# Performance work log

Hardware: AMD Instinct MI355X
Metric: run time of the kernel (lower is better)

Reference implementation:

```python
import jax, jax.numpy as jnp
import numpy as np

NUM_HEADS = 16
HEAD_DIM = 128  # embed_dim 2048 / 16 heads


def setup_inputs() -> dict:
    key = jax.random.key(0)
    x = jax.random.normal(key, (2, 2048, 2048), dtype=jnp.float32)
    return {"x": x}


def reference(x):
    # EvoAttn forward: V-only causal self-attention (q = k = v = reshaped x).
    B, L, E = x.shape
    H, D = NUM_HEADS, HEAD_DIM
    v = x.reshape(B, L, H, D).transpose(0, 2, 1, 3)  # (B, H, L, D)
    scale = 1.0 / jnp.sqrt(jnp.asarray(D, dtype=x.dtype))
    scores = jnp.einsum("bhqd,bhkd->bhqk", v, v) * scale  # (B, H, L, L)
    causal = jnp.tril(jnp.ones((L, L), dtype=bool))
    scores = jnp.where(causal[None, None], scores, jnp.asarray(-jnp.inf, dtype=scores.dtype))
    p = jax.nn.softmax(scores, axis=-1)
    y = jnp.einsum("bhqk,bhkd->bhqd", p, v)  # (B, H, L, D)
    return y.transpose(0, 2, 1, 3).reshape(B, L, E)
```

## Files before the change

kernel.cpp:

```cpp
#include <hip/hip_runtime.h>
#include <hip/hip_bf16.h>


#define TL 2048
#define TE 2048
#define TD 128
#define KB 64
#define NTILES 32
#define TILE_B 16384
#define KV_REGION (32 * NTILES * TILE_B)
#define WS_NEED (2u * (unsigned)KV_REGION)

typedef __attribute__((ext_vector_type(8))) short bf16x8;
typedef __attribute__((ext_vector_type(4))) float f32x4;
typedef __attribute__((ext_vector_type(8))) unsigned short u16x8;
typedef __attribute__((ext_vector_type(4))) unsigned short u16x4;

#define SCALE_LOG2E 0.12751879f

__device__ __forceinline__ unsigned short f2bf(float f) {
  __hip_bfloat16 h = __float2bfloat16(f);
  return __builtin_bit_cast(unsigned short, h);
}

__device__ __forceinline__ f32x4 mfma16(bf16x8 a, bf16x8 b, f32x4 c) {
  return __builtin_amdgcn_mfma_f32_16x16x32_bf16(a, b, c, 0, 0, 0);
}

__device__ __forceinline__ void gl_lds16(const void* g, void* l) {
  __builtin_amdgcn_global_load_lds(
      (__attribute__((address_space(1))) void*)(g),
      (__attribute__((address_space(3))) void*)(l), 16, 0, 0);
}

__global__ void __launch_bounds__(256)
prepack(const float* __restrict__ x, char* __restrict__ wsb) {
  const int bid = blockIdx.x;
  const int kt = bid & 31;
  const int bh = bid >> 5;
  const int b = bh >> 4;
  const int h = bh & 15;
  const float* src = x + (size_t)b * TL * TE + h * TD + (size_t)kt * KB * TE;
  const int t = threadIdx.x;
  const int kr = (t >> 4) << 2;
  const int d0 = (t & 15) << 3;
  unsigned short c[4][8];
#pragma unroll
  for (int rr = 0; rr < 4; ++rr) {
    const float* p = src + (kr + rr) * TE + d0;
    const float4 a = *(const float4*)p;
    const float4 bb = *(const float4*)(p + 4);
    c[rr][0] = f2bf(a.x);  c[rr][1] = f2bf(a.y);  c[rr][2] = f2bf(a.z);  c[rr][3] = f2bf(a.w);
    c[rr][4] = f2bf(bb.x); c[rr][5] = f2bf(bb.y); c[rr][6] = f2bf(bb.z); c[rr][7] = f2bf(bb.w);
  }
  char* gkv = wsb + (size_t)bid * TILE_B;
  const int kt2 = kr >> 4;
  const int q0r = kr & 15;
  const int cc_ = (t & 15) >> 2;
  const int gg_ = (t & 15) & 3;
#pragma unroll
  for (int rr = 0; rr < 4; ++rr) {
    u16x8 o = {c[rr][0], c[rr][1], c[rr][2], c[rr][3],
               c[rr][4], c[rr][5], c[rr][6], c[rr][7]};
    const int off = (((kt2 * 4 + cc_) * 64 + gg_ * 16 + (q0r + rr)) << 4);
    *(u16x8*)(gkv + off) = o;
  }
  char* gkt = wsb + KV_REGION + (size_t)bid * TILE_B;
  const int half = kr >> 5;
  const int g = (kr >> 3) & 3;
  const int j0 = kr & 7;
#pragma unroll
  for (int cc = 0; cc < 8; ++cc) {
    const int d = d0 + cc;
    u16x4 o = {c[0][cc], c[1][cc], c[2][cc], c[3][cc]};
    const int off = (((half * 8 + (d >> 4)) * 64 + g * 16 + (d & 15)) << 4) + j0 * 2;
    *(u16x4*)(gkt + off) = o;
  }
}

__global__ void __launch_bounds__(256)
evo_attn2(const char* __restrict__ wsb, float* __restrict__ out) {
  __shared__ char smem[3 * TILE_B + 8192];

  const int t = threadIdx.x;
  const int lane = t & 63;
  const int w = t >> 6;
  const int g = lane >> 4;
  const int q15 = lane & 15;

  const int blk = blockIdx.x;
  const int bh = (blk & 7) * 4 + (blk >> 7);
  const int a = (blk >> 3) & 15;
  const int b = bh >> 4;
  const int h = bh & 15;

  const char* gkv = wsb + (size_t)bh * (NTILES * TILE_B);
  const char* gkt = wsb + KV_REGION + (size_t)bh * (NTILES * TILE_B);
  char* plw = smem + 3 * TILE_B + w * 2048;
  const char* kvtb = smem + 2 * TILE_B;
  const int l16 = lane * 16;

#define STAGE_KV(BUFI, KT)                                                 \
  {                                                                        \
    char* dst_ = smem + (BUFI) * TILE_B + (t >> 6) * 1024;                 \
    const char* src_ = gkv + (size_t)(KT) * TILE_B + t * 16;               \
    _Pragma("unroll")                                                      \
    for (int i_ = 0; i_ < 4; ++i_) gl_lds16(src_ + i_ * 4096, dst_ + i_ * 4096); \
  }
#define STAGE_KVT(KT)                                                      \
  {                                                                        \
    char* dst_ = smem + 2 * TILE_B + (t >> 6) * 1024;                      \
    const char* src_ = gkt + (size_t)(KT) * TILE_B + t * 16;               \
    _Pragma("unroll")                                                      \
    for (int i_ = 0; i_ < 4; ++i_) gl_lds16(src_ + i_ * 4096, dst_ + i_ * 4096); \
  }

#pragma unroll 1
  for (int seg = 0; seg < 2; ++seg) {
    const int qt = seg ? (31 - a) : a;
    const int nt = qt + 1;

    STAGE_KV(0, qt);
    if (nt > 1) STAGE_KV(1, 0);
    STAGE_KVT(qt);
    asm volatile("s_waitcnt vmcnt(0)" ::: "memory");
    __builtin_amdgcn_s_barrier();
    asm volatile("" ::: "memory");

    bf16x8 qf[4];
#pragma unroll
    for (int c = 0; c < 4; ++c)
      qf[c] = *(const bf16x8*)(smem + (w * 4 + c) * 1024 + l16);

    f32x4 acc[8];
#pragma unroll
    for (int dt = 0; dt < 8; ++dt) acc[dt] = (f32x4){0.f, 0.f, 0.f, 0.f};
    float mrun = -1e30f;
    float lrun = 0.f;

    for (int s = 0; s < nt; ++s) {
      if (s > 0) {
        asm volatile("s_waitcnt vmcnt(8)" ::: "memory");
        __builtin_amdgcn_s_barrier();
        asm volatile("" ::: "memory");
      }
      const char* kv = smem + (s & 1) * TILE_B;

      float sv[16];
      __builtin_amdgcn_s_setprio(1);
#pragma unroll
      for (int kt2 = 0; kt2 < 4; ++kt2) {
        f32x4 st = (f32x4){0.f, 0.f, 0.f, 0.f};
#pragma unroll
        for (int c = 0; c < 4; ++c) {
          bf16x8 kf = *(const bf16x8*)(kv + (kt2 * 4 + c) * 1024 + l16);
          st = mfma16(kf, qf[c], st);
        }
#pragma unroll
        for (int r = 0; r < 4; ++r) sv[kt2 * 4 + r] = st[r];
      }
      __builtin_amdgcn_s_setprio(0);

      if (s == 0) {
        const int qrel = 16 * w + q15;
#pragma unroll
        for (int kt2 = 0; kt2 < 4; ++kt2)
#pragma unroll
          for (int r = 0; r < 4; ++r)
            if (kt2 * 16 + g * 4 + r > qrel) sv[kt2 * 4 + r] = -1e30f;
      }

      float m0 = fmaxf(fmaxf(sv[0], sv[1]), fmaxf(sv[2], sv[3]));
      float m1 = fmaxf(fmaxf(sv[4], sv[5]), fmaxf(sv[6], sv[7]));
      float m2 = fmaxf(fmaxf(sv[8], sv[9]), fmaxf(sv[10], sv[11]));
      float m3 = fmaxf(fmaxf(sv[12], sv[13]), fmaxf(sv[14], sv[15]));
      float tmax = fmaxf(fmaxf(m0, m1), fmaxf(m2, m3));
      tmax = fmaxf(tmax, __shfl_xor(tmax, 16));
      tmax = fmaxf(tmax, __shfl_xor(tmax, 32));

      float pf[16];
      if (__all(tmax <= mrun)) {
        const float nmc = -mrun * SCALE_LOG2E;
#pragma unroll
        for (int i = 0; i < 16; ++i) pf[i] = exp2f(fmaf(sv[i], SCALE_LOG2E, nmc));
      } else {
        const float mnew = fmaxf(mrun, tmax);
        const float al = exp2f((mrun - mnew) * SCALE_LOG2E);
        mrun = mnew;
        const float nmc = -mnew * SCALE_LOG2E;
#pragma unroll
        for (int i = 0; i < 16; ++i) pf[i] = exp2f(fmaf(sv[i], SCALE_LOG2E, nmc));
        lrun *= al;
        float ar[4];
#pragma unroll
        for (int r = 0; r < 4; ++r) ar[r] = __shfl(al, g * 4 + r);
#pragma unroll
        for (int dt = 0; dt < 8; ++dt)
#pragma unroll
          for (int r = 0; r < 4; ++r) acc[dt][r] *= ar[r];
      }
      {
        float s01 = (pf[0] + pf[1]) + (pf[2] + pf[3]);
        float s23 = (pf[4] + pf[5]) + (pf[6] + pf[7]);
        float s45 = (pf[8] + pf[9]) + (pf[10] + pf[11]);
        float s67 = (pf[12] + pf[13]) + (pf[14] + pf[15]);
        lrun += (s01 + s23) + (s45 + s67);
      }

      {
        const int wb = q15 * 16 + (g & 1) * 8;
#pragma unroll
        for (int kt2 = 0; kt2 < 4; ++kt2) {
          u16x4 o = {f2bf(pf[kt2 * 4]), f2bf(pf[kt2 * 4 + 1]),
                     f2bf(pf[kt2 * 4 + 2]), f2bf(pf[kt2 * 4 + 3])};
          *(u16x4*)(plw + (kt2 * 2 + (g >> 1)) * 256 + wb) = o;
        }
      }
      asm volatile("s_waitcnt lgkmcnt(0)" ::: "memory");

      if (s > 0) {
        if (s + 1 < nt) asm volatile("s_waitcnt vmcnt(4)" ::: "memory");
        else            asm volatile("s_waitcnt vmcnt(0)" ::: "memory");
        __builtin_amdgcn_s_barrier();
        asm volatile("" ::: "memory");
      }

      bf16x8 pa0 = *(const bf16x8*)(plw + g * 256 + q15 * 16);
      bf16x8 pa1 = *(const bf16x8*)(plw + (4 + g) * 256 + q15 * 16);
      __builtin_amdgcn_s_setprio(1);
#pragma unroll
      for (int dt = 0; dt < 8; ++dt) {
        bf16x8 vb0 = *(const bf16x8*)(kvtb + dt * 1024 + l16);
        bf16x8 vb1 = *(const bf16x8*)(kvtb + (8 + dt) * 1024 + l16);
        acc[dt] = mfma16(pa0, vb0, acc[dt]);
        acc[dt] = mfma16(pa1, vb1, acc[dt]);
      }
      __builtin_amdgcn_s_setprio(0);

      __builtin_amdgcn_s_barrier();
      asm volatile("" ::: "memory");
      if (s + 1 < nt) STAGE_KVT(s);
      if (s + 2 < nt) STAGE_KV(s & 1, s + 1);
    }

    lrun += __shfl_xor(lrun, 16);
    lrun += __shfl_xor(lrun, 32);
    const float inv = 1.f / lrun;
    float ir[4];
#pragma unroll
    for (int r = 0; r < 4; ++r) ir[r] = __shfl(inv, g * 4 + r);

    float* ob = out + ((size_t)b * TL + qt * 64 + 16 * w) * TE + h * TD;
#pragma unroll
    for (int dt = 0; dt < 8; ++dt)
#pragma unroll
      for (int r = 0; r < 4; ++r)
        ob[(g * 4 + r) * TE + dt * 16 + q15] = acc[dt][r] * ir[r];

    __builtin_amdgcn_s_barrier();
    asm volatile("" ::: "memory");
  }
}

__device__ __forceinline__ bf16x8 ld256s(const unsigned short* base, int row, int inrow) {
  const int off = (row * 256 + inrow) ^ ((row & 7) << 4);
  return *(const bf16x8*)((const char*)base + off);
}
__device__ __forceinline__ bf16x8 ld128s(const unsigned short* base, int row, int inrow) {
  const int off = (row * 128 + inrow) ^ ((row & 7) << 4);
  return *(const bf16x8*)((const char*)base + off);
}

__device__ __forceinline__ void stage_tile_fb(const float* __restrict__ src,
                                              unsigned short* kv, unsigned short* kvt,
                                              int t) {
  const int kr = (t >> 4) << 2;
  const int d0 = (t & 15) << 3;
  unsigned short c[4][8];
#pragma unroll
  for (int rr = 0; rr < 4; ++rr) {
    const float* p = src + (kr + rr) * TE + d0;
    const float4 a = *(const float4*)p;
    const float4 b = *(const float4*)(p + 4);
    c[rr][0] = f2bf(a.x); c[rr][1] = f2bf(a.y); c[rr][2] = f2bf(a.z); c[rr][3] = f2bf(a.w);
    c[rr][4] = f2bf(b.x); c[rr][5] = f2bf(b.y); c[rr][6] = f2bf(b.z); c[rr][7] = f2bf(b.w);
  }
#pragma unroll
  for (int rr = 0; rr < 4; ++rr) {
    const int r = kr + rr;
    u16x8 o = {c[rr][0], c[rr][1], c[rr][2], c[rr][3],
               c[rr][4], c[rr][5], c[rr][6], c[rr][7]};
    const int off = (r * 256 + d0 * 2) ^ ((r & 7) << 4);
    *(u16x8*)((char*)kv + off) = o;
  }
#pragma unroll
  for (int cc = 0; cc < 8; ++cc) {
    const int d = d0 + cc;
    u16x4 o = {c[0][cc], c[1][cc], c[2][cc], c[3][cc]};
    const int off = (d * 128 + kr * 2) ^ ((d & 7) << 4);
    *(u16x4*)((char*)kvt + off) = o;
  }
}

__global__ void __launch_bounds__(256)
evo_attn(const float* __restrict__ x, float* __restrict__ out) {
  __shared__ unsigned short kv[KB * TD];
  __shared__ unsigned short kvt[TD * KB];
  __shared__ unsigned short pl[4 * 16 * KB];

  const int t = threadIdx.x;
  const int lane = t & 63;
  const int w = t >> 6;
  const int g = lane >> 4;
  const int q15 = lane & 15;

  const int bh = blockIdx.x & 31;
  const int qt = 31 - (blockIdx.x >> 5);
  const int b = bh >> 4;
  const int h = bh & 15;
  const float* xb = x + (size_t)b * TL * TE + h * TD;
  const int q0 = qt * KB;

  stage_tile_fb(xb + (size_t)q0 * TE, kv, kvt, t);
  __syncthreads();

  bf16x8 qf[4];
#pragma unroll
  for (int c = 0; c < 4; ++c)
    qf[c] = ld256s(kv, 16 * w + q15, c * 64 + g * 16);

  f32x4 acc[8];
#pragma unroll
  for (int dt = 0; dt < 8; ++dt) acc[dt] = (f32x4){0.f, 0.f, 0.f, 0.f};
  float mrun = -1e30f;
  float lrun = 0.f;
  unsigned short* plw = pl + w * (16 * KB);

  for (int s = 0; s <= qt; ++s) {
    if (s > 0) {
      __syncthreads();
      stage_tile_fb(xb + (size_t)(s - 1) * KB * TE, kv, kvt, t);
      __syncthreads();
    }
    float sv[16];
#pragma unroll
    for (int kt2 = 0; kt2 < 4; ++kt2) {
      f32x4 st = (f32x4){0.f, 0.f, 0.f, 0.f};
#pragma unroll
      for (int c = 0; c < 4; ++c) {
        bf16x8 kf = ld256s(kv, kt2 * 16 + q15, c * 64 + g * 16);
        st = mfma16(kf, qf[c], st);
      }
#pragma unroll
      for (int r = 0; r < 4; ++r) sv[kt2 * 4 + r] = st[r] * SCALE_LOG2E;
    }
    if (s == 0) {
      const int qrel = 16 * w + q15;
#pragma unroll
      for (int kt2 = 0; kt2 < 4; ++kt2)
#pragma unroll
        for (int r = 0; r < 4; ++r)
          if (kt2 * 16 + g * 4 + r > qrel) sv[kt2 * 4 + r] = -1e30f;
    }
    float tmax = sv[0];
#pragma unroll
    for (int i = 1; i < 16; ++i) tmax = fmaxf(tmax, sv[i]);
    tmax = fmaxf(tmax, __shfl_xor(tmax, 16));
    tmax = fmaxf(tmax, __shfl_xor(tmax, 32));
    const float mnew = fmaxf(mrun, tmax);
    const float al = exp2f(mrun - mnew);
    mrun = mnew;
    float psum = 0.f;
    unsigned short pb[16];
#pragma unroll
    for (int i = 0; i < 16; ++i) {
      const float p = exp2f(sv[i] - mnew);
      psum += p;
      pb[i] = f2bf(p);
    }
    lrun = lrun * al + psum;
#pragma unroll
    for (int kt2 = 0; kt2 < 4; ++kt2) {
      u16x4 o = {pb[kt2 * 4], pb[kt2 * 4 + 1], pb[kt2 * 4 + 2], pb[kt2 * 4 + 3]};
      const int off = (q15 * 128 + kt2 * 32 + g * 8) ^ ((q15 & 7) << 4);
      *(u16x4*)((char*)plw + off) = o;
    }
    asm volatile("s_waitcnt lgkmcnt(0)" ::: "memory");
    float ar[4];
#pragma unroll
    for (int r = 0; r < 4; ++r) ar[r] = __shfl(al, g * 4 + r);
#pragma unroll
    for (int dt = 0; dt < 8; ++dt)
#pragma unroll
      for (int r = 0; r < 4; ++r) acc[dt][r] *= ar[r];
    bf16x8 pa0 = ld128s(plw, q15, g * 16);
    bf16x8 pa1 = ld128s(plw, q15, 64 + g * 16);
#pragma unroll
    for (int dt = 0; dt < 8; ++dt) {
      bf16x8 vb0 = ld128s(kvt, dt * 16 + q15, g * 16);
      bf16x8 vb1 = ld128s(kvt, dt * 16 + q15, 64 + g * 16);
      acc[dt] = mfma16(pa0, vb0, acc[dt]);
      acc[dt] = mfma16(pa1, vb1, acc[dt]);
    }
  }

  lrun += __shfl_xor(lrun, 16);
  lrun += __shfl_xor(lrun, 32);
  const float inv = 1.f / lrun;
  float ir[4];
#pragma unroll
  for (int r = 0; r < 4; ++r) ir[r] = __shfl(inv, g * 4 + r);
  float* ob = out + ((size_t)b * TL + q0 + 16 * w) * TE + h * TD;
#pragma unroll
  for (int dt = 0; dt < 8; ++dt)
#pragma unroll
    for (int r = 0; r < 4; ++r)
      ob[(g * 4 + r) * TE + dt * 16 + q15] = acc[dt][r] * ir[r];
}

extern "C" void kernel_launch(void* const* d_in, const int* in_sizes, int n_in,
                              void* d_out, int out_size, void* d_ws, size_t ws_size,
                              hipStream_t stream) {
  const float* x = (const float*)d_in[0];
  float* out = (float*)d_out;
  (void)in_sizes; (void)n_in; (void)out_size;
  if (ws_size >= (size_t)WS_NEED) {
    char* wsb = (char*)d_ws;
    prepack<<<dim3(1024), dim3(256), 0, stream>>>(x, wsb);
    evo_attn2<<<dim3(512), dim3(256), 0, stream>>>(wsb, out);
  } else {
    evo_attn<<<dim3(1024), dim3(256), 0, stream>>>(x, out);
  }
}
```

Measured before the change: 92.71 us.

## Double-buffer transposed V tiles and cut per-iteration barriers to one

Gives the transposed-V (KVT) tile its own double buffer so it is staged together with the K/V tile one iteration ahead. This removes the two mid-iteration waitcnt+barrier pairs and the end-of-segment barrier, leaving a single vmcnt(0)+barrier after the PV MFMAs. The aim is less synchronisation stall and more overlap of global-to-LDS copies with compute. In exchange, LDS per block grows by one 16 KB tile, and the wait becomes a full vmcnt(0) rather than a partial drain.

After: 92.45 us. Within noise of the previous version (-0.3%).

```diff
diff --git a/kernel.cpp b/kernel.cpp
--- a/kernel.cpp
+++ b/kernel.cpp
@@ -79,8 +79,8 @@
 }
 
 __global__ void __launch_bounds__(256)
-evo_attn2(const char* __restrict__ wsb, float* __restrict__ out) {
-  __shared__ char smem[3 * TILE_B + 8192];
+evo_attn8(const char* __restrict__ wsb, float* __restrict__ out) {
+  __shared__ char smem[4 * TILE_B + 8192];
 
   const int t = threadIdx.x;
   const int lane = t & 63;
@@ -96,8 +96,7 @@
 
   const char* gkv = wsb + (size_t)bh * (NTILES * TILE_B);
   const char* gkt = wsb + KV_REGION + (size_t)bh * (NTILES * TILE_B);
-  char* plw = smem + 3 * TILE_B + w * 2048;
-  const char* kvtb = smem + 2 * TILE_B;
+  char* plw = smem + 4 * TILE_B + w * 2048;
   const int l16 = lane * 16;
 
 #define STAGE_KV(BUFI, KT)                                                 \
@@ -107,13 +106,15 @@
     _Pragma("unroll")                                                      \
     for (int i_ = 0; i_ < 4; ++i_) gl_lds16(src_ + i_ * 4096, dst_ + i_ * 4096); \
   }
-#define STAGE_KVT(KT)                                                      \
+#define STAGE_KVT(BUFI, KT)                                                \
   {                                                                        \
-    char* dst_ = smem + 2 * TILE_B + (t >> 6) * 1024;                      \
+    char* dst_ = smem + (2 + (BUFI)) * TILE_B + (t >> 6) * 1024;           \
     const char* src_ = gkt + (size_t)(KT) * TILE_B + t * 16;               \
     _Pragma("unroll")                                                      \
     for (int i_ = 0; i_ < 4; ++i_) gl_lds16(src_ + i_ * 4096, dst_ + i_ * 4096); \
   }
+
+#define TIDX(S) (((S) == 0) ? qt : ((S)-1))
 
 #pragma unroll 1
   for (int seg = 0; seg < 2; ++seg) {
@@ -121,9 +122,10 @@
     const int nt = qt + 1;
 
     STAGE_KV(0, qt);
-    if (nt > 1) STAGE_KV(1, 0);
-    STAGE_KVT(qt);
-    asm volatile("s_waitcnt vmcnt(0)" ::: "memory");
+    STAGE_KVT(0, qt);
+    if (nt > 1) { STAGE_KV(1, 0); STAGE_KVT(1, 0); }
+    if (nt > 1) asm volatile("s_waitcnt vmcnt(8)" ::: "memory");
+    else        asm volatile("s_waitcnt vmcnt(0)" ::: "memory");
     __builtin_amdgcn_s_barrier();
     asm volatile("" ::: "memory");
 
@@ -139,14 +141,10 @@
     float lrun = 0.f;
 
     for (int s = 0; s < nt; ++s) {
-      if (s > 0) {
-        asm volatile("s_waitcnt vmcnt(8)" ::: "memory");
-        __builtin_amdgcn_s_barrier();
-        asm volatile("" ::: "memory");
-      }
       const char* kv = smem + (s & 1) * TILE_B;
-
-      float sv[16];
+      const char* kvtb = smem + (2 + (s & 1)) * TILE_B;
+
+      float pf[16];
       __builtin_amdgcn_s_setprio(1);
 #pragma unroll
       for (int kt2 = 0; kt2 < 4; ++kt2) {
@@ -157,7 +155,7 @@
           st = mfma16(kf, qf[c], st);
         }
 #pragma unroll
-        for (int r = 0; r < 4; ++r) sv[kt2 * 4 + r] = st[r];
+        for (int r = 0; r < 4; ++r) pf[kt2 * 4 + r] = st[r];
       }
       __builtin_amdgcn_s_setprio(0);
 
@@ -167,29 +165,28 @@
         for (int kt2 = 0; kt2 < 4; ++kt2)
 #pragma unroll
           for (int r = 0; r < 4; ++r)
-            if (kt2 * 16 + g * 4 + r > qrel) sv[kt2 * 4 + r] = -1e30f;
-      }
-
-      float m0 = fmaxf(fmaxf(sv[0], sv[1]), fmaxf(sv[2], sv[3]));
-      float m1 = fmaxf(fmaxf(sv[4], sv[5]), fmaxf(sv[6], sv[7]));
-      float m2 = fmaxf(fmaxf(sv[8], sv[9]), fmaxf(sv[10], sv[11]));
-      float m3 = fmaxf(fmaxf(sv[12], sv[13]), fmaxf(sv[14], sv[15]));
+            if (kt2 * 16 + g * 4 + r > qrel) pf[kt2 * 4 + r] = -1e30f;
+      }
+
+      float m0 = fmaxf(fmaxf(pf[0], pf[1]), fmaxf(pf[2], pf[3]));
+      float m1 = fmaxf(fmaxf(pf[4], pf[5]), fmaxf(pf[6], pf[7]));
+      float m2 = fmaxf(fmaxf(pf[8], pf[9]), fmaxf(pf[10], pf[11]));
+      float m3 = fmaxf(fmaxf(pf[12], pf[13]), fmaxf(pf[14], pf[15]));
       float tmax = fmaxf(fmaxf(m0, m1), fmaxf(m2, m3));
       tmax = fmaxf(tmax, __shfl_xor(tmax, 16));
       tmax = fmaxf(tmax, __shfl_xor(tmax, 32));
 
-      float pf[16];
       if (__all(tmax <= mrun)) {
         const float nmc = -mrun * SCALE_LOG2E;
 #pragma unroll
-        for (int i = 0; i < 16; ++i) pf[i] = exp2f(fmaf(sv[i], SCALE_LOG2E, nmc));
+        for (int i = 0; i < 16; ++i) pf[i] = exp2f(fmaf(pf[i], SCALE_LOG2E, nmc));
       } else {
         const float mnew = fmaxf(mrun, tmax);
         const float al = exp2f((mrun - mnew) * SCALE_LOG2E);
         mrun = mnew;
         const float nmc = -mnew * SCALE_LOG2E;
 #pragma unroll
-        for (int i = 0; i < 16; ++i) pf[i] = exp2f(fmaf(sv[i], SCALE_LOG2E, nmc));
+        for (int i = 0; i < 16; ++i) pf[i] = exp2f(fmaf(pf[i], SCALE_LOG2E, nmc));
         lrun *= al;
         float ar[4];
 #pragma unroll
@@ -218,13 +215,6 @@
       }
       asm volatile("s_waitcnt lgkmcnt(0)" ::: "memory");
 
-      if (s > 0) {
-        if (s + 1 < nt) asm volatile("s_waitcnt vmcnt(4)" ::: "memory");
-        else            asm volatile("s_waitcnt vmcnt(0)" ::: "memory");
-        __builtin_amdgcn_s_barrier();
-        asm volatile("" ::: "memory");
-      }
-
       bf16x8 pa0 = *(const bf16x8*)(plw + g * 256 + q15 * 16);
       bf16x8 pa1 = *(const bf16x8*)(plw + (4 + g) * 256 + q15 * 16);
       __builtin_amdgcn_s_setprio(1);
@@ -237,10 +227,13 @@
       }
       __builtin_amdgcn_s_setprio(0);
 
+      if (s + 1 < nt) asm volatile("s_waitcnt vmcnt(0)" ::: "memory");
       __builtin_amdgcn_s_barrier();
       asm volatile("" ::: "memory");
-      if (s + 1 < nt) STAGE_KVT(s);
-      if (s + 2 < nt) STAGE_KV(s & 1, s + 1);
+      if (s + 2 < nt) {
+        STAGE_KV(s & 1, s + 1);
+        STAGE_KVT(s & 1, s + 1);
+      }
     }
 
     lrun += __shfl_xor(lrun, 16);
@@ -256,9 +249,6 @@
 #pragma unroll
       for (int r = 0; r < 4; ++r)
         ob[(g * 4 + r) * TE + dt * 16 + q15] = acc[dt][r] * ir[r];
-
-    __builtin_amdgcn_s_barrier();
-    asm volatile("" ::: "memory");
   }
 }
 
@@ -427,7 +417,7 @@
   if (ws_size >= (size_t)WS_NEED) {
     char* wsb = (char*)d_ws;
     prepack<<<dim3(1024), dim3(256), 0, stream>>>(x, wsb);
-    evo_attn2<<<dim3(512), dim3(256), 0, stream>>>(wsb, out);
+    evo_attn8<<<dim3(512), dim3(256), 0, stream>>>(wsb, out);
   } else {
     evo_attn<<<dim3(1024), dim3(256), 0, stream>>>(x, out);
   }
```
